# Performance work log

Hardware: AMD Instinct MI355X
Metric: run time of the kernel (lower is better)

Reference implementation:

```python
import jax, jax.numpy as jnp
import numpy as np

B, T, H, K = 16, 2048, 512, 15
FIRE_TH = 1.0
SMOOTH = 1.0
NOISE_TH = 0.0
LN_EPS = 1e-5


def setup_inputs() -> dict:
    key = jax.random.key(0)
    ks = jax.random.split(key, 8)
    s = lambda n: 1.0 / np.sqrt(n)
    return {
        "x": jax.random.normal(ks[0], (B, T, H), jnp.float32),
        "x_lens": jax.random.randint(ks[1], (B,), T // 2, T + 1),
        "pw1_w": jax.random.normal(ks[2], (2 * H, H), jnp.float32) * s(H),
        "pw1_b": jnp.zeros((2 * H,), jnp.float32),
        "dw_w": jax.random.normal(ks[3], (H, K), jnp.float32) * s(K),
        "dw_b": jnp.zeros((H,), jnp.float32),
        "ln_g": jnp.ones((H,), jnp.float32),
        "ln_b": jnp.zeros((H,), jnp.float32),
        "pw2_w": jax.random.normal(ks[4], (H, H), jnp.float32) * s(H),
        "pw2_b": jnp.zeros((H,), jnp.float32),
        "lin_w": jax.random.normal(ks[5], (H,), jnp.float32) * s(H),
        "lin_b": jnp.zeros((), jnp.float32),
    }


def _layer_norm(x, g, b):
    m = x.mean(-1, keepdims=True)
    v = ((x - m) ** 2).mean(-1, keepdims=True)
    return (x - m) * jax.lax.rsqrt(v + LN_EPS) * g + b


def _swish(x):
    return x * jax.nn.sigmoid(x)


def _conv_module(x, pw1_w, pw1_b, dw_w, dw_b, ln_g, ln_b, pw2_w, pw2_b):
    # wenet ConvolutionModule (causal, layer_norm): pw-conv -> GLU -> causal depthwise -> LN -> swish -> pw-conv
    h = jnp.einsum('bth,oh->bto', x, pw1_w) + pw1_b          # (B,T,2H)
    h = h[..., :H] * jax.nn.sigmoid(h[..., H:])              # GLU over channel halves
    hp = jnp.pad(h, ((0, 0), (K - 1, 0), (0, 0)))            # causal left pad
    rhs = dw_w.T[:, None, :]                                 # (K, 1, H) depthwise kernel
    h = jax.lax.conv_general_dilated(
        hp, rhs, window_strides=(1,), padding='VALID',
        dimension_numbers=('NWC', 'WIO', 'NWC'),
        feature_group_count=H) + dw_b                        # (B,T,H)
    h = _swish(_layer_norm(h, ln_g, ln_b))
    return jnp.einsum('bth,oh->bto', h, pw2_w) + pw2_b


def _cif_scan(x, alphas):
    # sequential integrate-and-fire over time, batched over B
    def step(carry, inp):
        integrate, frame = carry
        alpha, xt = inp                                       # (B,), (B,H)
        dist = FIRE_TH - integrate
        integrate = integrate + alpha
        fire = integrate >= FIRE_TH
        cur = jnp.where(fire, dist, alpha)
        remain = alpha - cur
        frame_acc = frame + cur[:, None] * xt
        new_frame = jnp.where(fire[:, None], remain[:, None] * xt, frame_acc)
        new_int = jnp.where(fire, integrate - FIRE_TH, integrate)
        return (new_int, new_frame), (integrate, frame_acc)
    init = (jnp.zeros((B,), x.dtype), jnp.zeros((B, H), x.dtype))
    _, (fires, frames) = jax.lax.scan(step, init, (alphas.T, x.transpose(1, 0, 2)))
    return fires.T, frames.transpose(1, 0, 2)                 # (B,T), (B,T,H)


def _gather_fired(fires, frames):
    # ragged gather of fired frames into a fixed (B,T,H) padded buffer
    mask = fires >= FIRE_TH                                   # (B,T)
    dest = jnp.where(mask, jnp.cumsum(mask, axis=1) - 1, T)   # dump non-fired to slot T
    out = jnp.zeros((B, T + 1, H), frames.dtype)
    out = out.at[jnp.arange(B)[:, None], dest].set(frames)
    fired = out[:, :T]
    return fired, jnp.flip(fired, axis=-1)                    # torch.flip(dims=[1]) flips hidden dim


def reference(x, x_lens, pw1_w, pw1_b, dw_w, dw_b, ln_g, ln_b, pw2_w, pw2_b, lin_w, lin_b):
    mask = (jnp.arange(T)[None, :] < x_lens[:, None]).astype(x.dtype)   # (B,T)
    hidden = _conv_module(x, pw1_w, pw1_b, dw_w, dw_b, ln_g, ln_b, pw2_w, pw2_b)
    logits = jnp.einsum('bth,h->bt', hidden, lin_w) + lin_b
    alphas = jax.nn.relu(jax.nn.sigmoid(logits) * SMOOTH - NOISE_TH) * mask
    predicted_token_nums = alphas.sum(-1)
    fires, frames = _cif_scan(x, alphas)
    fired_frames, r_fired_frames = _gather_fired(fires, frames)
    return fired_frames, predicted_token_nums, r_fired_frames
```

## Files before the change

kernel.cpp:

```cpp
#include <hip/hip_runtime.h>
#include <math.h>

#define B_ 16
#define T_ 2048
#define H_ 512
#define K_ 15
#define M_ (B_*T_)

typedef __attribute__((ext_vector_type(8))) short short8;
typedef __attribute__((ext_vector_type(4))) float f32x4;

__device__ __forceinline__ unsigned short f2bf(float f) {
  union { float f; unsigned u; } v; v.f = f;
  unsigned r = v.u + 0x7FFFu + ((v.u >> 16) & 1u);
  return (unsigned short)(r >> 16);
}
__device__ __forceinline__ float bf2f(unsigned short b) {
  union { float f; unsigned u; } v; v.u = ((unsigned)b) << 16;
  return v.f;
}

__device__ __forceinline__ void async_load16(const void* g, void* l) {
  __builtin_amdgcn_global_load_lds((const __attribute__((address_space(1))) void*)g,
                                   (__attribute__((address_space(3))) void*)l, 16, 0, 0);
}

__global__ void convx_k(const float* __restrict__ x, unsigned short* __restrict__ hi,
                        unsigned short* __restrict__ lo, int n4) {
  int i = blockIdx.x * blockDim.x + threadIdx.x;
  int stride = gridDim.x * blockDim.x;
  for (; i < n4; i += stride) {
    float4 v = ((const float4*)x)[i];
    ushort4 h, l;
    h.x = f2bf(v.x); l.x = f2bf(v.x - bf2f(h.x));
    h.y = f2bf(v.y); l.y = f2bf(v.y - bf2f(h.y));
    h.z = f2bf(v.z); l.z = f2bf(v.z - bf2f(h.z));
    h.w = f2bf(v.w); l.w = f2bf(v.w - bf2f(h.w));
    ((ushort4*)hi)[i] = h;
    ((ushort4*)lo)[i] = l;
  }
}

__global__ __launch_bounds__(256) void weff_k(const float* __restrict__ pw2_w,
    const float* __restrict__ lin_w, float* __restrict__ weff) {
  __shared__ float red[256];
  int h = blockIdx.x * 64 + (threadIdx.x & 63);
  int og = threadIdx.x >> 6;
  float acc = 0.f;
  for (int o = og * 128; o < og * 128 + 128; ++o) acc += pw2_w[o * H_ + h] * lin_w[o];
  red[threadIdx.x] = acc;
  __syncthreads();
  if (threadIdx.x < 64)
    weff[h] = red[threadIdx.x] + red[threadIdx.x + 64] + red[threadIdx.x + 128] + red[threadIdx.x + 192];
}

__global__ void beff_k(const float* __restrict__ pw2_b, const float* __restrict__ lin_w,
                       const float* __restrict__ lin_b, float* __restrict__ weff) {
  __shared__ float red[512];
  int h = threadIdx.x;
  red[h] = pw2_b[h] * lin_w[h];
  __syncthreads();
  for (int s = 256; s > 0; s >>= 1) {
    if (h < s) red[h] += red[h + s];
    __syncthreads();
  }
  if (h == 0) weff[H_] = red[0] + lin_b[0];
}

__global__ __launch_bounds__(256) void gemm_mfma_k(
    const unsigned short* __restrict__ Ahi, const unsigned short* __restrict__ Alo,
    const unsigned short* __restrict__ Whi, const unsigned short* __restrict__ Wlo,
    const float* __restrict__ bias, float* __restrict__ g) {
  __shared__ short As[128 * 64];
  __shared__ short Bs[128 * 64];
  const int tid = threadIdx.x;
  const int m0 = blockIdx.x * 128;
  const int n0 = blockIdx.y * 64;
  const int w = tid >> 6;
  const int lane = tid & 63;

  f32x4 acc[2][8];
#pragma unroll
  for (int mt = 0; mt < 2; ++mt)
#pragma unroll
    for (int nt = 0; nt < 8; ++nt) acc[mt][nt] = (f32x4){0.f, 0.f, 0.f, 0.f};

  const unsigned short* Aptr[3] = {Ahi, Alo, Ahi};
  const unsigned short* Bptr[3] = {Whi, Whi, Wlo};

  const int srow[4] = {(0 * 256 + tid) >> 3, (1 * 256 + tid) >> 3,
                       (2 * 256 + tid) >> 3, (3 * 256 + tid) >> 3};
  const int scc = tid & 7;

  for (int p = 0; p < 3; ++p) {
    const unsigned short* Ab = Aptr[p];
    const unsigned short* Bb = Bptr[p];
#pragma unroll 1
    for (int kk = 0; kk < 8; ++kk) {
      const int k0 = kk * 64;
      __syncthreads();
#pragma unroll
      for (int j = 0; j < 4; ++j) {
        int row = srow[j];
        int csrc = scc ^ (row & 7);
        int lbase = __builtin_amdgcn_readfirstlane((j * 256 + w * 64) * 8);
        async_load16(Ab + (size_t)(m0 + row) * 512 + k0 + csrc * 8, &As[lbase]);
        int wrow = (row < 64) ? (n0 + row) : (n0 + 448 + row);
        async_load16(Bb + (size_t)wrow * 512 + k0 + csrc * 8, &Bs[lbase]);
      }
      __syncthreads();
#pragma unroll
      for (int ks = 0; ks < 2; ++ks) {
        const int swz = (ks * 4 + (lane >> 4)) ^ (lane & 7);
        const int rA = w * 32 + (lane & 15);
        const int rB = lane & 15;
        short8 af[2], bfr[8];
#pragma unroll
        for (int mt = 0; mt < 2; ++mt)
          af[mt] = *(const short8*)&As[((rA + mt * 16) * 8 + swz) * 8];
#pragma unroll
        for (int nt = 0; nt < 8; ++nt)
          bfr[nt] = *(const short8*)&Bs[((rB + nt * 16) * 8 + swz) * 8];
#pragma unroll
        for (int mt = 0; mt < 2; ++mt)
#pragma unroll
          for (int nt = 0; nt < 8; ++nt)
            acc[mt][nt] = __builtin_amdgcn_mfma_f32_16x16x32_bf16(af[mt], bfr[nt], acc[mt][nt], 0, 0, 0);
      }
    }
  }

  const int col = lane & 15, rq = lane >> 4;
#pragma unroll
  for (int mt = 0; mt < 2; ++mt) {
#pragma unroll
    for (int nt = 0; nt < 4; ++nt) {
      int gcol = n0 + nt * 16 + col;
      float ba = bias[gcol];
      float bg = bias[512 + gcol];
#pragma unroll
      for (int r = 0; r < 4; ++r) {
        int grow = m0 + w * 32 + mt * 16 + rq * 4 + r;
        float a = acc[mt][nt][r] + ba;
        float gt = acc[mt][nt + 4][r] + bg;
        g[(size_t)grow * 512 + gcol] = a / (1.f + expf(-gt));
      }
    }
  }
}

__global__ __launch_bounds__(512) void conv_ln_k(const float* __restrict__ g,
    const float* __restrict__ dw_w, const float* __restrict__ dw_b,
    const float* __restrict__ ln_g, const float* __restrict__ ln_b,
    const float* __restrict__ weff, const int* __restrict__ x_lens,
    float* __restrict__ aT) {
  __shared__ float wlds[H_ * K_];
  __shared__ float red1[16][8];
  __shared__ float red2[16][8];
  __shared__ float mvs[16], rss[16];
  const int tid = threadIdx.x;
  const int c = tid;
  const int t0 = blockIdx.x * 16;
  const int b = blockIdx.y;

  for (int i = tid; i < H_ * K_; i += 512) wlds[i] = dw_w[i];
  __syncthreads();

  const float* gb = g + ((size_t)b * T_) * H_ + c;
  float gv[30];
#pragma unroll
  for (int i = 0; i < 30; ++i) {
    int t = t0 - 14 + i;
    gv[i] = (t >= 0) ? gb[(size_t)t * H_] : 0.f;
  }
  float wreg[15];
#pragma unroll
  for (int k = 0; k < 15; ++k) wreg[k] = wlds[c * 15 + k];
  float dwb = dw_b[c];
  float h2[16];
#pragma unroll
  for (int j = 0; j < 16; ++j) {
    float s = dwb;
#pragma unroll
    for (int k = 0; k < 15; ++k) s += gv[j + k] * wreg[k];
    h2[j] = s;
  }
  const int lane = tid & 63, wid = tid >> 6;
#pragma unroll
  for (int j = 0; j < 16; ++j) {
    float s1 = h2[j], s2 = h2[j] * h2[j];
#pragma unroll
    for (int off = 32; off > 0; off >>= 1) {
      s1 += __shfl_down(s1, off, 64);
      s2 += __shfl_down(s2, off, 64);
    }
    if (lane == 0) { red1[j][wid] = s1; red2[j][wid] = s2; }
  }
  __syncthreads();
  if (tid < 16) {
    float s1 = 0.f, s2 = 0.f;
#pragma unroll
    for (int w = 0; w < 8; ++w) { s1 += red1[tid][w]; s2 += red2[tid][w]; }
    float m = s1 * (1.f / 512.f);
    float v = s2 * (1.f / 512.f) - m * m;
    mvs[tid] = m;
    rss[tid] = rsqrtf(v + 1e-5f);
  }
  __syncthreads();
  float lg = ln_g[c], lb = ln_b[c], we = weff[c];
#pragma unroll
  for (int j = 0; j < 16; ++j) {
    float y = (h2[j] - mvs[j]) * rss[j] * lg + lb;
    float sw = y / (1.f + expf(-y));
    float p = sw * we;
#pragma unroll
    for (int off = 32; off > 0; off >>= 1) p += __shfl_down(p, off, 64);
    if (lane == 0) red1[j][wid] = p;
  }
  __syncthreads();
  if (tid < 16) {
    float s = 0.f;
#pragma unroll
    for (int w = 0; w < 8; ++w) s += red1[tid][w];
    float logit = s + weff[H_];
    float a = 1.f / (1.f + expf(-logit));
    int t = t0 + tid;
    if (t >= x_lens[b]) a = 0.f;
    aT[t * B_ + b] = a;
  }
}

__global__ __launch_bounds__(64) void cif_p1_k(const float* __restrict__ aT,
                                               float* __restrict__ chk) {
  const int b = threadIdx.x;
  if (b >= B_) return;
  const float* ar = aT + b;
  float integ = 0.f;
  float bufA[32], bufB[32];
#pragma unroll
  for (int j = 0; j < 32; ++j) bufA[j] = ar[j * B_];
#pragma unroll 1
  for (int s = 0; s < 64; s += 2) {
#pragma unroll
    for (int j = 0; j < 32; ++j) bufB[j] = ar[((s + 1) * 32 + j) * B_];
    chk[s * B_ + b] = integ;
#pragma unroll
    for (int j = 0; j < 32; ++j) {
      float ni = integ + bufA[j];
      integ = ni - floorf(ni);
    }
    if (s + 2 < 64) {
#pragma unroll
      for (int j = 0; j < 32; ++j) bufA[j] = ar[((s + 2) * 32 + j) * B_];
    }
    chk[(s + 1) * B_ + b] = integ;
#pragma unroll
    for (int j = 0; j < 32; ++j) {
      float ni = integ + bufB[j];
      integ = ni - floorf(ni);
    }
  }
}

__global__ __launch_bounds__(64) void cif_p2_k(const float* __restrict__ aT,
    const float* __restrict__ chk, float* __restrict__ wdT, float* __restrict__ wrT,
    int* __restrict__ fire_pos, int* __restrict__ nfires, float* __restrict__ tok) {
  const int b = blockIdx.x;
  const int seg = threadIdx.x;
  const int t0 = seg * 32;
  float integ = chk[seg * B_ + b];
  float a[32];
#pragma unroll
  for (int j = 0; j < 32; ++j) a[j] = aT[(t0 + j) * B_ + b];
  unsigned fmask = 0u;
  float ssum = 0.f;
#pragma unroll
  for (int j = 0; j < 32; ++j) {
    float al = a[j];
    float dist = 1.0f - integ;
    float ni = integ + al;
    bool fire = ni >= 1.0f;
    float cur = fire ? dist : al;
    wdT[(t0 + j) * B_ + b] = cur;
    wrT[(t0 + j) * B_ + b] = al - cur;
    if (fire) fmask |= (1u << j);
    integ = ni - floorf(ni);
    ssum += al;
  }
  const int cnt = __popc(fmask);
  int incl = cnt;
#pragma unroll
  for (int off = 1; off < 64; off <<= 1) {
    int v = __shfl_up(incl, off, 64);
    if (seg >= off) incl += v;
  }
  int idx = incl - cnt;
  unsigned m = fmask;
  while (m) {
    int j = __ffs(m) - 1;
    m &= m - 1;
    fire_pos[b * T_ + idx++] = t0 + j;
  }
  if (seg == 63) nfires[b] = incl;
#pragma unroll
  for (int off = 32; off > 0; off >>= 1) ssum += __shfl_down(ssum, off, 64);
  if (seg == 0) tok[b] = ssum;
}

__global__ __launch_bounds__(128) void frames_k(const float* __restrict__ x,
    const float* __restrict__ aT, const float* __restrict__ wdT,
    const float* __restrict__ wrT, const int* __restrict__ fire_pos,
    const int* __restrict__ nfires, float* __restrict__ out0, float* __restrict__ out2) {
  const int b = blockIdx.y;
  const int j = blockIdx.x;
  const int h = threadIdx.x << 2;
  const size_t ob = ((size_t)b * T_ + j) * H_;
  if (j >= nfires[b]) {
    float4 z = make_float4(0.f, 0.f, 0.f, 0.f);
    *(float4*)(out0 + ob + h) = z;
    *(float4*)(out2 + ob + h) = z;
    return;
  }
  const int te = fire_pos[b * T_ + j];
  const int ts = (j > 0) ? fire_pos[b * T_ + j - 1] : -1;
  const float* xb = x + ((size_t)b * T_) * H_;
  float4 acc = make_float4(0.f, 0.f, 0.f, 0.f);
  if (j > 0) {
    float w = wrT[ts * B_ + b];
    float4 xv = *(const float4*)(xb + (size_t)ts * H_ + h);
    acc.x = w * xv.x; acc.y = w * xv.y; acc.z = w * xv.z; acc.w = w * xv.w;
  }
  for (int t = ts + 1; t < te; ++t) {
    float w = aT[t * B_ + b];
    float4 xv = *(const float4*)(xb + (size_t)t * H_ + h);
    acc.x += w * xv.x; acc.y += w * xv.y; acc.z += w * xv.z; acc.w += w * xv.w;
  }
  {
    float w = wdT[te * B_ + b];
    float4 xv = *(const float4*)(xb + (size_t)te * H_ + h);
    acc.x += w * xv.x; acc.y += w * xv.y; acc.z += w * xv.z; acc.w += w * xv.w;
  }
  *(float4*)(out0 + ob + h) = acc;
  float4 racc = make_float4(acc.w, acc.z, acc.y, acc.x);
  *(float4*)(out2 + ob + (H_ - 4 - h)) = racc;
}

extern "C" void kernel_launch(void* const* d_in, const int* in_sizes, int n_in,
                              void* d_out, int out_size, void* d_ws, size_t ws_size,
                              hipStream_t stream) {
  const float* x     = (const float*)d_in[0];
  const int*   xlens = (const int*)d_in[1];
  const float* pw1_w = (const float*)d_in[2];
  const float* pw1_b = (const float*)d_in[3];
  const float* dw_w  = (const float*)d_in[4];
  const float* dw_b  = (const float*)d_in[5];
  const float* ln_g  = (const float*)d_in[6];
  const float* ln_b  = (const float*)d_in[7];
  const float* pw2_w = (const float*)d_in[8];
  const float* pw2_b = (const float*)d_in[9];
  const float* lin_w = (const float*)d_in[10];
  const float* lin_b = (const float*)d_in[11];

  float* out0 = (float*)d_out;
  float* tok  = out0 + (size_t)B_ * T_ * H_;
  float* out2 = tok + B_;

  char* ws = (char*)d_ws;
  float* g             = (float*)ws;
  unsigned short* Ahi  = (unsigned short*)(ws + (size_t)M_ * H_ * 4);
  unsigned short* Alo  = Ahi + (size_t)M_ * H_;
  unsigned short* Whi  = Alo + (size_t)M_ * H_;
  unsigned short* Wlo  = Whi + (size_t)2 * H_ * H_;
  float* aT       = (float*)(Wlo + (size_t)2 * H_ * H_);
  float* wdT      = aT + B_ * T_;
  float* wrT      = wdT + B_ * T_;
  int*   fire_pos = (int*)(wrT + B_ * T_);
  int*   nfires   = fire_pos + B_ * T_;
  float* weff     = (float*)(nfires + 64);
  float* chk      = weff + 1024;

  convx_k<<<2048, 256, 0, stream>>>(x, Ahi, Alo, M_ * H_ / 4);
  convx_k<<<256, 256, 0, stream>>>(pw1_w, Whi, Wlo, 2 * H_ * H_ / 4);
  weff_k<<<8, 256, 0, stream>>>(pw2_w, lin_w, weff);
  beff_k<<<1, 512, 0, stream>>>(pw2_b, lin_w, lin_b, weff);
  gemm_mfma_k<<<dim3(256, 8), 256, 0, stream>>>(Ahi, Alo, Whi, Wlo, pw1_b, g);
  conv_ln_k<<<dim3(128, 16), 512, 0, stream>>>(g, dw_w, dw_b, ln_g, ln_b, weff, xlens, aT);
  cif_p1_k<<<1, 64, 0, stream>>>(aT, chk);
  cif_p2_k<<<16, 64, 0, stream>>>(aT, chk, wdT, wrT, fire_pos, nfires, tok);
  frames_k<<<dim3(2048, 16), 128, 0, stream>>>(x, aT, wdT, wrT, fire_pos, nfires, out0, out2);
}
```

Before: 497.7 us.

## Fuse split-bf16 passes in GEMM, widen conv-LN time tile, merge bias kernel

```diff
diff --git a/kernel.cpp b/kernel.cpp
--- a/kernel.cpp
+++ b/kernel.cpp
@@ -42,108 +42,122 @@
 }
 
 __global__ __launch_bounds__(256) void weff_k(const float* __restrict__ pw2_w,
-    const float* __restrict__ lin_w, float* __restrict__ weff) {
+    const float* __restrict__ pw2_b, const float* __restrict__ lin_w,
+    const float* __restrict__ lin_b, float* __restrict__ weff) {
   __shared__ float red[256];
-  int h = blockIdx.x * 64 + (threadIdx.x & 63);
-  int og = threadIdx.x >> 6;
-  float acc = 0.f;
-  for (int o = og * 128; o < og * 128 + 128; ++o) acc += pw2_w[o * H_ + h] * lin_w[o];
-  red[threadIdx.x] = acc;
-  __syncthreads();
-  if (threadIdx.x < 64)
-    weff[h] = red[threadIdx.x] + red[threadIdx.x + 64] + red[threadIdx.x + 128] + red[threadIdx.x + 192];
-}
-
-__global__ void beff_k(const float* __restrict__ pw2_b, const float* __restrict__ lin_w,
-                       const float* __restrict__ lin_b, float* __restrict__ weff) {
-  __shared__ float red[512];
-  int h = threadIdx.x;
-  red[h] = pw2_b[h] * lin_w[h];
-  __syncthreads();
-  for (int s = 256; s > 0; s >>= 1) {
-    if (h < s) red[h] += red[h + s];
-    __syncthreads();
-  }
-  if (h == 0) weff[H_] = red[0] + lin_b[0];
+  if (blockIdx.x < 8) {
+    int h = blockIdx.x * 64 + (threadIdx.x & 63);
+    int og = threadIdx.x >> 6;
+    float acc = 0.f;
+    for (int o = og * 128; o < og * 128 + 128; ++o) acc += pw2_w[o * H_ + h] * lin_w[o];
+    red[threadIdx.x] = acc;
+    __syncthreads();
+    if (threadIdx.x < 64)
+      weff[h] = red[threadIdx.x] + red[threadIdx.x + 64] + red[threadIdx.x + 128] + red[threadIdx.x + 192];
+  } else {
+    int i = threadIdx.x;
+    red[i] = pw2_b[i] * lin_w[i] + pw2_b[i + 256] * lin_w[i + 256];
+    __syncthreads();
+    for (int s = 128; s > 0; s >>= 1) {
+      if (i < s) red[i] += red[i + s];
+      __syncthreads();
+    }
+    if (i == 0) weff[H_] = red[0] + lin_b[0];
+  }
 }
 
 __global__ __launch_bounds__(256) void gemm_mfma_k(
     const unsigned short* __restrict__ Ahi, const unsigned short* __restrict__ Alo,
     const unsigned short* __restrict__ Whi, const unsigned short* __restrict__ Wlo,
     const float* __restrict__ bias, float* __restrict__ g) {
-  __shared__ short As[128 * 64];
-  __shared__ short Bs[128 * 64];
+  __shared__ short Ah[128 * 32];
+  __shared__ short Al[128 * 32];
+  __shared__ short Bh[128 * 32];
+  __shared__ short Bl[128 * 32];
   const int tid = threadIdx.x;
   const int m0 = blockIdx.x * 128;
   const int n0 = blockIdx.y * 64;
-  const int w = tid >> 6;
-  const int lane = tid & 63;
-
-  f32x4 acc[2][8];
-#pragma unroll
-  for (int mt = 0; mt < 2; ++mt)
-#pragma unroll
-    for (int nt = 0; nt < 8; ++nt) acc[mt][nt] = (f32x4){0.f, 0.f, 0.f, 0.f};
-
-  const unsigned short* Aptr[3] = {Ahi, Alo, Ahi};
-  const unsigned short* Bptr[3] = {Whi, Whi, Wlo};
-
-  const int srow[4] = {(0 * 256 + tid) >> 3, (1 * 256 + tid) >> 3,
-                       (2 * 256 + tid) >> 3, (3 * 256 + tid) >> 3};
-  const int scc = tid & 7;
-
-  for (int p = 0; p < 3; ++p) {
-    const unsigned short* Ab = Aptr[p];
-    const unsigned short* Bb = Bptr[p];
+  const int w = tid >> 6, lane = tid & 63;
+  const int wr = w >> 1, wc = w & 1;
+
+  f32x4 acc[4][4];
+#pragma unroll
+  for (int mt = 0; mt < 4; ++mt)
+#pragma unroll
+    for (int nt = 0; nt < 4; ++nt) acc[mt][nt] = (f32x4){0.f, 0.f, 0.f, 0.f};
+
+  int offA[2], offB[2], ldsb[2];
+#pragma unroll
+  for (int j = 0; j < 2; ++j) {
+    int L = j * 256 + tid;
+    int r = L >> 2;
+    int csrc = (L & 3) ^ ((r >> 1) & 3);
+    offA[j] = (m0 + r) * 512 + csrc * 8;
+    int wrow = (r < 64) ? (n0 + r) : (n0 + 448 + r);
+    offB[j] = wrow * 512 + csrc * 8;
+    ldsb[j] = __builtin_amdgcn_readfirstlane((j * 256 + w * 64) * 16);
+  }
+
+  const int q = lane >> 4;
+  int aAddr[4], bAddr[4];
+#pragma unroll
+  for (int mt = 0; mt < 4; ++mt) {
+    int rA = wr * 64 + mt * 16 + (lane & 15);
+    aAddr[mt] = rA * 64 + (q ^ ((rA >> 1) & 3)) * 16;
+  }
+#pragma unroll
+  for (int nt = 0; nt < 4; ++nt) {
+    int rB = (nt >> 1) * 64 + wc * 32 + (nt & 1) * 16 + (lane & 15);
+    bAddr[nt] = rB * 64 + (q ^ ((rB >> 1) & 3)) * 16;
+  }
+
 #pragma unroll 1
-    for (int kk = 0; kk < 8; ++kk) {
-      const int k0 = kk * 64;
-      __syncthreads();
-#pragma unroll
-      for (int j = 0; j < 4; ++j) {
-        int row = srow[j];
-        int csrc = scc ^ (row & 7);
-        int lbase = __builtin_amdgcn_readfirstlane((j * 256 + w * 64) * 8);
-        async_load16(Ab + (size_t)(m0 + row) * 512 + k0 + csrc * 8, &As[lbase]);
-        int wrow = (row < 64) ? (n0 + row) : (n0 + 448 + row);
-        async_load16(Bb + (size_t)wrow * 512 + k0 + csrc * 8, &Bs[lbase]);
+  for (int kk = 0; kk < 16; ++kk) {
+    const int k0 = kk * 32;
+    __syncthreads();
+#pragma unroll
+    for (int j = 0; j < 2; ++j) {
+      async_load16(Ahi + offA[j] + k0, (char*)Ah + ldsb[j]);
+      async_load16(Alo + offA[j] + k0, (char*)Al + ldsb[j]);
+      async_load16(Whi + offB[j] + k0, (char*)Bh + ldsb[j]);
+      async_load16(Wlo + offB[j] + k0, (char*)Bl + ldsb[j]);
+    }
+    __syncthreads();
+    short8 ah[4], al[4], bh[4], bl[4];
+#pragma unroll
+    for (int mt = 0; mt < 4; ++mt) {
+      ah[mt] = *(const short8*)((const char*)Ah + aAddr[mt]);
+      al[mt] = *(const short8*)((const char*)Al + aAddr[mt]);
+    }
+#pragma unroll
+    for (int nt = 0; nt < 4; ++nt) {
+      bh[nt] = *(const short8*)((const char*)Bh + bAddr[nt]);
+      bl[nt] = *(const short8*)((const char*)Bl + bAddr[nt]);
+    }
+#pragma unroll
+    for (int mt = 0; mt < 4; ++mt)
+#pragma unroll
+      for (int nt = 0; nt < 4; ++nt) {
+        acc[mt][nt] = __builtin_amdgcn_mfma_f32_16x16x32_bf16(ah[mt], bh[nt], acc[mt][nt], 0, 0, 0);
+        acc[mt][nt] = __builtin_amdgcn_mfma_f32_16x16x32_bf16(al[mt], bh[nt], acc[mt][nt], 0, 0, 0);
+        acc[mt][nt] = __builtin_amdgcn_mfma_f32_16x16x32_bf16(ah[mt], bl[nt], acc[mt][nt], 0, 0, 0);
       }
-      __syncthreads();
-#pragma unroll
-      for (int ks = 0; ks < 2; ++ks) {
-        const int swz = (ks * 4 + (lane >> 4)) ^ (lane & 7);
-        const int rA = w * 32 + (lane & 15);
-        const int rB = lane & 15;
-        short8 af[2], bfr[8];
-#pragma unroll
-        for (int mt = 0; mt < 2; ++mt)
-          af[mt] = *(const short8*)&As[((rA + mt * 16) * 8 + swz) * 8];
-#pragma unroll
-        for (int nt = 0; nt < 8; ++nt)
-          bfr[nt] = *(const short8*)&Bs[((rB + nt * 16) * 8 + swz) * 8];
-#pragma unroll
-        for (int mt = 0; mt < 2; ++mt)
-#pragma unroll
-          for (int nt = 0; nt < 8; ++nt)
-            acc[mt][nt] = __builtin_amdgcn_mfma_f32_16x16x32_bf16(af[mt], bfr[nt], acc[mt][nt], 0, 0, 0);
-      }
-    }
   }
 
   const int col = lane & 15, rq = lane >> 4;
 #pragma unroll
-  for (int mt = 0; mt < 2; ++mt) {
-#pragma unroll
-    for (int nt = 0; nt < 4; ++nt) {
-      int gcol = n0 + nt * 16 + col;
+  for (int mt = 0; mt < 4; ++mt) {
+#pragma unroll
+    for (int ntp = 0; ntp < 2; ++ntp) {
+      int gcol = n0 + wc * 32 + ntp * 16 + col;
       float ba = bias[gcol];
       float bg = bias[512 + gcol];
 #pragma unroll
       for (int r = 0; r < 4; ++r) {
-        int grow = m0 + w * 32 + mt * 16 + rq * 4 + r;
-        float a = acc[mt][nt][r] + ba;
-        float gt = acc[mt][nt + 4][r] + bg;
-        g[(size_t)grow * 512 + gcol] = a / (1.f + expf(-gt));
+        int m = m0 + wr * 64 + mt * 16 + rq * 4 + r;
+        float a = acc[mt][ntp][r] + ba;
+        float gt = acc[mt][2 + ntp][r] + bg;
+        g[(size_t)m * 512 + gcol] = a / (1.f + expf(-gt));
       }
     }
   }
@@ -155,78 +169,88 @@
     const float* __restrict__ weff, const int* __restrict__ x_lens,
     float* __restrict__ aT) {
   __shared__ float wlds[H_ * K_];
-  __shared__ float red1[16][8];
-  __shared__ float red2[16][8];
+  __shared__ float tbuf[16][512];
   __shared__ float mvs[16], rss[16];
   const int tid = threadIdx.x;
   const int c = tid;
-  const int t0 = blockIdx.x * 16;
+  const int t0 = blockIdx.x * 64;
   const int b = blockIdx.y;
 
   for (int i = tid; i < H_ * K_; i += 512) wlds[i] = dw_w[i];
-  __syncthreads();
-
+  const int xlen = x_lens[b];
   const float* gb = g + ((size_t)b * T_) * H_ + c;
-  float gv[30];
+
+  float gwin[30];
 #pragma unroll
   for (int i = 0; i < 30; ++i) {
     int t = t0 - 14 + i;
-    gv[i] = (t >= 0) ? gb[(size_t)t * H_] : 0.f;
-  }
+    gwin[i] = (t >= 0) ? gb[(size_t)t * H_] : 0.f;
+  }
+  __syncthreads();
   float wreg[15];
 #pragma unroll
   for (int k = 0; k < 15; ++k) wreg[k] = wlds[c * 15 + k];
-  float dwb = dw_b[c];
-  float h2[16];
-#pragma unroll
-  for (int j = 0; j < 16; ++j) {
-    float s = dwb;
-#pragma unroll
-    for (int k = 0; k < 15; ++k) s += gv[j + k] * wreg[k];
-    h2[j] = s;
-  }
-  const int lane = tid & 63, wid = tid >> 6;
-#pragma unroll
-  for (int j = 0; j < 16; ++j) {
-    float s1 = h2[j], s2 = h2[j] * h2[j];
-#pragma unroll
-    for (int off = 32; off > 0; off >>= 1) {
-      s1 += __shfl_down(s1, off, 64);
-      s2 += __shfl_down(s2, off, 64);
-    }
-    if (lane == 0) { red1[j][wid] = s1; red2[j][wid] = s2; }
-  }
-  __syncthreads();
-  if (tid < 16) {
+  const float dwb = dw_b[c], lg = ln_g[c], lb = ln_b[c], we = weff[c];
+  const float beff = weff[H_];
+  const int tt = tid >> 5, p = tid & 31;
+
+#pragma unroll 1
+  for (int qc = 0; qc < 4; ++qc) {
+    float h2[16];
+#pragma unroll
+    for (int j = 0; j < 16; ++j) {
+      float s = dwb;
+#pragma unroll
+      for (int k = 0; k < 15; ++k) s += gwin[j + k] * wreg[k];
+      h2[j] = s;
+      tbuf[j][c] = s;
+    }
+    __syncthreads();
     float s1 = 0.f, s2 = 0.f;
 #pragma unroll
-    for (int w = 0; w < 8; ++w) { s1 += red1[tid][w]; s2 += red2[tid][w]; }
-    float m = s1 * (1.f / 512.f);
-    float v = s2 * (1.f / 512.f) - m * m;
-    mvs[tid] = m;
-    rss[tid] = rsqrtf(v + 1e-5f);
-  }
-  __syncthreads();
-  float lg = ln_g[c], lb = ln_b[c], we = weff[c];
-#pragma unroll
-  for (int j = 0; j < 16; ++j) {
-    float y = (h2[j] - mvs[j]) * rss[j] * lg + lb;
-    float sw = y / (1.f + expf(-y));
-    float p = sw * we;
-#pragma unroll
-    for (int off = 32; off > 0; off >>= 1) p += __shfl_down(p, off, 64);
-    if (lane == 0) red1[j][wid] = p;
-  }
-  __syncthreads();
-  if (tid < 16) {
+    for (int k = 0; k < 16; ++k) {
+      float v = tbuf[tt][k * 32 + p];
+      s1 += v; s2 += v * v;
+    }
+#pragma unroll
+    for (int off = 16; off > 0; off >>= 1) {
+      s1 += __shfl_down(s1, off, 32);
+      s2 += __shfl_down(s2, off, 32);
+    }
+    if (p == 0) {
+      float m = s1 * (1.f / 512.f);
+      float v = s2 * (1.f / 512.f) - m * m;
+      mvs[tt] = m;
+      rss[tt] = rsqrtf(v + 1e-5f);
+    }
+    __syncthreads();
+#pragma unroll
+    for (int j = 0; j < 16; ++j) {
+      float y = (h2[j] - mvs[j]) * rss[j] * lg + lb;
+      float sw = y / (1.f + expf(-y));
+      tbuf[j][c] = sw * we;
+    }
+    __syncthreads();
     float s = 0.f;
 #pragma unroll
-    for (int w = 0; w < 8; ++w) s += red1[tid][w];
-    float logit = s + weff[H_];
-    float a = 1.f / (1.f + expf(-logit));
-    int t = t0 + tid;
-    if (t >= x_lens[b]) a = 0.f;
-    aT[t * B_ + b] = a;
+    for (int k = 0; k < 16; ++k) s += tbuf[tt][k * 32 + p];
+#pragma unroll
+    for (int off = 16; off > 0; off >>= 1) s += __shfl_down(s, off, 32);
+    if (p == 0) {
+      float logit = s + beff;
+      float a = 1.f / (1.f + expf(-logit));
+      int t = t0 + qc * 16 + tt;
+      if (t >= xlen) a = 0.f;
+      aT[t * B_ + b] = a;
+    }
+    if (qc < 3) {
+#pragma unroll
+      for (int i = 0; i < 14; ++i) gwin[i] = gwin[i + 16];
+#pragma unroll
+      for (int i = 0; i < 16; ++i)
+        gwin[14 + i] = gb[(size_t)(t0 + qc * 16 + 16 + i) * H_];
+    }
+    __syncthreads();
   }
 }
 
@@ -381,10 +405,9 @@
 
   convx_k<<<2048, 256, 0, stream>>>(x, Ahi, Alo, M_ * H_ / 4);
   convx_k<<<256, 256, 0, stream>>>(pw1_w, Whi, Wlo, 2 * H_ * H_ / 4);
-  weff_k<<<8, 256, 0, stream>>>(pw2_w, lin_w, weff);
-  beff_k<<<1, 512, 0, stream>>>(pw2_b, lin_w, lin_b, weff);
+  weff_k<<<9, 256, 0, stream>>>(pw2_w, pw2_b, lin_w, lin_b, weff);
   gemm_mfma_k<<<dim3(256, 8), 256, 0, stream>>>(Ahi, Alo, Whi, Wlo, pw1_b, g);
-  conv_ln_k<<<dim3(128, 16), 512, 0, stream>>>(g, dw_w, dw_b, ln_g, ln_b, weff, xlens, aT);
+  conv_ln_k<<<dim3(32, 16), 512, 0, stream>>>(g, dw_w, dw_b, ln_g, ln_b, weff, xlens, aT);
   cif_p1_k<<<1, 64, 0, stream>>>(aT, chk);
   cif_p2_k<<<16, 64, 0, stream>>>(aT, chk, wdT, wrT, fire_pos, nfires, tok);
   frames_k<<<dim3(2048, 16), 128, 0, stream>>>(x, aT, wdT, wrT, fire_pos, nfires, out0, out2);
```

Result: faster. 464.6 us (-6.6%).
